# Optimization experiments

Hardware: AMD Instinct MI355X
Metric: run time of the kernel (lower is better)

## Reference

```python
import jax, jax.numpy as jnp
import numpy as np

D_MODEL = 1024
N_HEADS = 16
SEQ_LEN = 2048
BATCH = 2
NEG = -1.0e9


def sinusoidal_embeddings(seq_len, d_k):
    # Faithful to the torch version: row 0 is all zeros; even cols get sin,
    # odd cols get cos of position/theta (theta uses the SAME index j, not j//2).
    theta = 10000.0 ** (2.0 * jnp.arange(d_k, dtype=jnp.float32) / d_k)  # [d_k]
    pos = jnp.arange(1, seq_len, dtype=jnp.float32)[:, None] / theta      # [S-1, d_k]
    even = (jnp.arange(d_k) % 2 == 0)
    body = jnp.where(even, jnp.sin(pos), jnp.cos(pos))                    # [S-1, d_k]
    return jnp.concatenate([jnp.zeros((1, d_k), dtype=pos.dtype), body], axis=0)


def setup_inputs() -> dict:
    key = jax.random.key(0)
    k_x, k_q, k_k, k_v, k_o = jax.random.split(key, 5)
    scale = 0.02
    return {
        "X": jax.random.normal(k_x, (BATCH, SEQ_LEN, D_MODEL), dtype=jnp.float32),
        "W_q": jax.random.normal(k_q, (D_MODEL, D_MODEL), dtype=jnp.float32) * scale,
        "W_k": jax.random.normal(k_k, (D_MODEL, D_MODEL), dtype=jnp.float32) * scale,
        "W_v": jax.random.normal(k_v, (D_MODEL, D_MODEL), dtype=jnp.float32) * scale,
        "W_o": jax.random.normal(k_o, (D_MODEL, D_MODEL), dtype=jnp.float32) * scale,
    }


def reference(X, W_q, W_k, W_v, W_o):
    B, S, D = X.shape
    H, d_k = N_HEADS, D // N_HEADS

    def proj(W):  # nn.Linear (no bias): y = x @ W.T, then split heads -> [B,H,S,d_k]
        return (X @ W.T).reshape(B, S, H, d_k).transpose(0, 2, 1, 3)

    Q, K, V = proj(W_q), proj(W_k), proj(W_v)

    pos = sinusoidal_embeddings(S, d_k)          # [S, d_k]
    Q = Q + pos
    K = K + pos

    mask = jnp.triu(jnp.full((S, S), NEG, dtype=X.dtype), k=1)  # [S,S]
    scores = jnp.einsum("bhqd,bhkd->bhqk", Q, K) / jnp.sqrt(jnp.float32(d_k)) + mask
    weights = jax.nn.softmax(scores, axis=-1)
    attn = jnp.einsum("bhqk,bhkd->bhqd", weights, V)            # [B,H,S,d_k]

    attn = attn.transpose(0, 2, 1, 3).reshape(B, S, D)
    return attn @ W_o.T + X
```

## Files before the change

### kernel.cpp

```cpp
#include <hip/hip_runtime.h>
#include <hip/hip_bf16.h>
#include <math.h>

#define S_LEN 2048
#define DMODEL 1024
#define NHEADS 16
#define DHEAD 64
#define NBATCH 2
#define MROWS (NBATCH * S_LEN)

typedef float f32x4 __attribute__((ext_vector_type(4)));
typedef unsigned short u16x8 __attribute__((ext_vector_type(8)));
typedef __bf16 bf16x8 __attribute__((ext_vector_type(8)));

__device__ __forceinline__ f32x4 mfma16(u16x8 a, u16x8 b, f32x4 c) {
    return __builtin_amdgcn_mfma_f32_16x16x32_bf16(
        __builtin_bit_cast(bf16x8, a), __builtin_bit_cast(bf16x8, b), c, 0, 0, 0);
}

__device__ __forceinline__ unsigned short f2bf(float f) {
    unsigned int u = __builtin_bit_cast(unsigned int, f);
    u += 0x7FFFu + ((u >> 16) & 1u);
    return (unsigned short)(u >> 16);
}

__device__ __forceinline__ unsigned int cvtpk(float lo, float hi) {
    unsigned int r;
    asm("v_cvt_pk_bf16_f32 %0, %1, %2" : "=v"(r) : "v"(lo), "v"(hi));
    return r;
}

__device__ __forceinline__ void gl16(const void* g, void* l) {
    __builtin_amdgcn_global_load_lds(
        (const __attribute__((address_space(1))) unsigned int*)g,
        (__attribute__((address_space(3))) unsigned int*)l, 16, 0, 0);
}

__global__ __launch_bounds__(256) void cvt5(
    const float* __restrict__ X, const float* __restrict__ Wq,
    const float* __restrict__ Wk, const float* __restrict__ Wv,
    const float* __restrict__ Wo,
    unsigned short* __restrict__ Xbf, unsigned short* __restrict__ Wbf,
    float* __restrict__ pos)
{
    int b = blockIdx.x;
    if (b >= 4096) {
        int i = (b - 4096) * 256 + threadIdx.x;
        int s = i >> 6, d = i & 63;
        float theta = powf(10000.0f, (2.0f * (float)d) / 64.0f);
        float x = (float)s / theta;
        float v = (d & 1) ? cosf(x) : sinf(x);
        pos[i] = (s == 0) ? 0.0f : v;
        return;
    }
    const float* s; unsigned short* d; int t;
    if (b < 2048) { s = X; d = Xbf; t = b * 256 + threadIdx.x; }
    else {
        int z = (b - 2048) >> 9, bb = (b - 2048) & 511;
        s = (z == 0) ? Wq : (z == 1) ? Wk : (z == 2) ? Wv : Wo;
        d = Wbf + (z << 20);
        t = bb * 256 + threadIdx.x;
    }
    float4 a = *((const float4*)s + t * 2);
    float4 c = *((const float4*)s + t * 2 + 1);
    u16x8 o;
    o[0] = f2bf(a.x); o[1] = f2bf(a.y); o[2] = f2bf(a.z); o[3] = f2bf(a.w);
    o[4] = f2bf(c.x); o[5] = f2bf(c.y); o[6] = f2bf(c.z); o[7] = f2bf(c.w);
    *((u16x8*)d + t) = o;
}

__global__ __launch_bounds__(128) void gemm_qkv(
    const unsigned short* __restrict__ Xbf, const unsigned short* __restrict__ Wbf,
    const float* __restrict__ pos,
    unsigned short* __restrict__ qb, unsigned short* __restrict__ kb,
    unsigned short* __restrict__ vt)
{
    const int y = blockIdx.y;
    const int z = y >> 4;
    const unsigned short* __restrict__ W = Wbf + (z << 20);
    __shared__ unsigned short As[128 * 64];
    __shared__ unsigned short Bs[64 * 64];
    const int t = threadIdx.x;
    const int lane = t & 63;
    const int w = t >> 6;
    const int m0 = blockIdx.x * 128;
    const int n0 = (y & 15) * 64;
    const int ll = lane & 15, lg = lane >> 4;
    const int r8 = lane >> 3, ch = (lane & 7) ^ r8;

    f32x4 acc[4][4] = {};

    const unsigned short* gA[8];
    const unsigned short* gB[4];
    #pragma unroll
    for (int i = 0; i < 8; i++) gA[i] = Xbf + (m0 + w * 64 + i * 8 + r8) * 1024 + ch * 8;
    #pragma unroll
    for (int i = 0; i < 4; i++) gB[i] = W + (n0 + w * 32 + i * 8 + r8) * 1024 + ch * 8;
    unsigned short* const dA = &As[(w * 64) * 64];
    unsigned short* const dB = &Bs[(w * 32) * 64];

    const int sw0 = ((0 * 4 + lg) ^ (ll & 7)) * 16;
    const int sw1 = ((1 * 4 + lg) ^ (ll & 7)) * 16;
    const char* const pA0 = (const char*)As + (w * 64 + ll) * 128 + sw0;
    const char* const pA1 = (const char*)As + (w * 64 + ll) * 128 + sw1;
    const char* const pB0 = (const char*)Bs + ll * 128 + sw0;
    const char* const pB1 = (const char*)Bs + ll * 128 + sw1;

    for (int k0 = 0; k0 < 1024; k0 += 64) {
        __syncthreads();
        #pragma unroll
        for (int i = 0; i < 8; i++) { gl16(gA[i], dA + i * 8 * 64); gA[i] += 64; }
        #pragma unroll
        for (int i = 0; i < 4; i++) { gl16(gB[i], dB + i * 8 * 64); gB[i] += 64; }
        __syncthreads();
        u16x8 af[4], bfv[4];
        #pragma unroll
        for (int m = 0; m < 4; m++) af[m] = *(const u16x8*)(pA0 + m * 2048);
        #pragma unroll
        for (int n = 0; n < 4; n++) bfv[n] = *(const u16x8*)(pB0 + n * 2048);
        __builtin_amdgcn_s_setprio(1);
        #pragma unroll
        for (int m = 0; m < 4; m++)
            #pragma unroll
            for (int n = 0; n < 4; n++)
                acc[m][n] = mfma16(af[m], bfv[n], acc[m][n]);
        __builtin_amdgcn_s_setprio(0);
        #pragma unroll
        for (int m = 0; m < 4; m++) af[m] = *(const u16x8*)(pA1 + m * 2048);
        #pragma unroll
        for (int n = 0; n < 4; n++) bfv[n] = *(const u16x8*)(pB1 + n * 2048);
        __builtin_amdgcn_s_setprio(1);
        #pragma unroll
        for (int m = 0; m < 4; m++)
            #pragma unroll
            for (int n = 0; n < 4; n++)
                acc[m][n] = mfma16(af[m], bfv[n], acc[m][n]);
        __builtin_amdgcn_s_setprio(0);
    }

    if (z == 2) {
        #pragma unroll
        for (int m = 0; m < 4; m++) {
            const int row0 = m0 + w * 64 + m * 16 + lg * 4;
            const int b = row0 >> 11, s0 = row0 & 2047;
            #pragma unroll
            for (int n = 0; n < 4; n++) {
                const int c = n0 + n * 16 + ll;
                const int h = c >> 6, d = c & 63;
                unsigned long long pk =
                    (unsigned long long)cvtpk(acc[m][n][0], acc[m][n][1]) |
                    ((unsigned long long)cvtpk(acc[m][n][2], acc[m][n][3]) << 32);
                *(unsigned long long*)&vt[(((b * NHEADS + h) * 64) + d) * S_LEN + s0] = pk;
            }
        }
    } else {
        unsigned short* const dst = (z == 0) ? qb : kb;
        #pragma unroll
        for (int m = 0; m < 4; m++) {
            #pragma unroll
            for (int n = 0; n < 4; n++) {
                #pragma unroll
                for (int r = 0; r < 4; r++) {
                    const int row = m0 + w * 64 + m * 16 + lg * 4 + r;
                    const int c = n0 + n * 16 + ll;
                    const int b = row >> 11, s = row & 2047;
                    const int h = c >> 6, d = c & 63;
                    float v = acc[m][n][r] + pos[s * 64 + d];
                    if (z == 0) v *= 0.1803368801111244f;
                    dst[(((b * NHEADS + h) * S_LEN) + s) * 64 + d] = f2bf(v);
                }
            }
        }
    }
}

__global__ __launch_bounds__(512, 4) void attn_kernel(
    const unsigned short* __restrict__ qb,
    const unsigned short* __restrict__ kb,
    const unsigned short* __restrict__ vt,
    unsigned short* __restrict__ attnb)
{
    __shared__ unsigned short Klds[2][64 * 64];
    __shared__ unsigned short Vlds[2][64 * 64];
    __shared__ unsigned short Plds[8][16 * 64];

    const int bh = blockIdx.y;
    const int x = blockIdx.x;
    const int qt = (bh < 16) ? (15 - x) : x;

    const int lane = threadIdx.x & 63;
    const int w = threadIdx.x >> 6;
    const int lg = lane >> 4, ll = lane & 15;
    const int r8 = lane >> 3, ch = (lane & 7) ^ r8;

    const unsigned short* Q = qb + bh * (S_LEN * 64);
    const unsigned short* K = kb + bh * (S_LEN * 64);
    const unsigned short* V = vt + bh * (64 * S_LEN);
    const int q0 = qt * 128 + w * 16;

    u16x8 qf0 = *(const u16x8*)(Q + (q0 + ll) * 64 + lg * 8);
    u16x8 qf1 = *(const u16x8*)(Q + (q0 + ll) * 64 + 32 + lg * 8);

    f32x4 o_acc[4] = {};
    float l_part = 0.0f;

    const int sw0 = ((0 * 4 + lg) ^ (ll & 7)) * 16;
    const int sw1 = ((1 * 4 + lg) ^ (ll & 7)) * 16;
    const int llb = ll * 128;
    const char* k0p0 = (const char*)&Klds[0][0] + llb + sw0;
    const char* k0p1 = (const char*)&Klds[0][0] + llb + sw1;
    const char* k1p0 = (const char*)&Klds[1][0] + llb + sw0;
    const char* k1p1 = (const char*)&Klds[1][0] + llb + sw1;
    const char* v0p0 = (const char*)&Vlds[0][0] + llb + sw0;
    const char* v0p1 = (const char*)&Vlds[0][0] + llb + sw1;
    const char* v1p0 = (const char*)&Vlds[1][0] + llb + sw0;
    const char* v1p1 = (const char*)&Vlds[1][0] + llb + sw1;
    const int E = (ll & 7) << 4;
    char* pwb = (char*)&Plds[w][0] + ((llb + lg * 8) ^ (E & 16));
    const int pw_o0 = 0 ^ (E & 96), pw_o1 = 32 ^ (E & 96);
    const int pw_o2 = 64 ^ (E & 96), pw_o3 = 96 ^ (E & 96);
    const char* pr0 = (const char*)&Plds[w][0] + llb + sw0;
    const char* pr1 = (const char*)&Plds[w][0] + llb + sw1;
    unsigned short* kd0 = &Klds[0][(w * 8) * 64];
    unsigned short* kd1 = &Klds[1][(w * 8) * 64];
    unsigned short* vd0 = &Vlds[0][(w * 8) * 64];
    unsigned short* vd1 = &Vlds[1][(w * 8) * 64];
    const unsigned short* gk = K + (w * 8 + r8) * 64 + ch * 8;
    const unsigned short* gv = V + (w * 8 + r8) * S_LEN + ch * 8;
    const int dthr = w * 16 + ll - lg * 4;

    auto stage2 = [&](unsigned short* kd, unsigned short* vd) {
        gl16(gk, kd);
        gl16(gv, vd);
        gk += 64 * 64;
        gv += 64;
    };

    auto tile_body = [&](const char* kp0, const char* kp1,
                         const char* vp0, const char* vp1, bool masked, int thr) {
        f32x4 sc[4] = {};
        __builtin_amdgcn_s_setprio(1);
        #pragma unroll
        for (int f = 0; f < 4; f++) {
            const u16x8 kfa = *(const u16x8*)(kp0 + f * 2048);
            sc[f] = mfma16(kfa, qf0, sc[f]);
            const u16x8 kfb = *(const u16x8*)(kp1 + f * 2048);
            sc[f] = mfma16(kfb, qf1, sc[f]);
        }
        __builtin_amdgcn_s_setprio(0);
        if (masked) {
            #pragma unroll
            for (int f = 0; f < 4; f++)
                #pragma unroll
                for (int r = 0; r < 4; r++)
                    if (f * 16 + r > thr) sc[f][r] = -1.0e9f;
        }
        float ts = 0.0f;
        #pragma unroll
        for (int f = 0; f < 4; f++)
            #pragma unroll
            for (int r = 0; r < 4; r++) {
                const float p = __builtin_amdgcn_exp2f(sc[f][r]);
                sc[f][r] = p;
                ts += p;
            }
        l_part += ts;
        *(unsigned long long*)(pwb + pw_o0) =
            (unsigned long long)cvtpk(sc[0][0], sc[0][1]) | ((unsigned long long)cvtpk(sc[0][2], sc[0][3]) << 32);
        *(unsigned long long*)(pwb + pw_o1) =
            (unsigned long long)cvtpk(sc[1][0], sc[1][1]) | ((unsigned long long)cvtpk(sc[1][2], sc[1][3]) << 32);
        *(unsigned long long*)(pwb + pw_o2) =
            (unsigned long long)cvtpk(sc[2][0], sc[2][1]) | ((unsigned long long)cvtpk(sc[2][2], sc[2][3]) << 32);
        *(unsigned long long*)(pwb + pw_o3) =
            (unsigned long long)cvtpk(sc[3][0], sc[3][1]) | ((unsigned long long)cvtpk(sc[3][2], sc[3][3]) << 32);
        const u16x8 pf0 = *(const u16x8*)pr0;
        const u16x8 pf1 = *(const u16x8*)pr1;
        __builtin_amdgcn_s_setprio(1);
        #pragma unroll
        for (int f = 0; f < 4; f++) {
            o_acc[f] = mfma16(pf0, *(const u16x8*)(vp0 + f * 2048), o_acc[f]);
            o_acc[f] = mfma16(pf1, *(const u16x8*)(vp1 + f * 2048), o_acc[f]);
        }
        __builtin_amdgcn_s_setprio(0);
    };

    stage2(kd0, vd0);

    for (int p = 0; p < qt; p++) {
        __syncthreads();
        stage2(kd1, vd1);
        tile_body(k0p0, k0p1, v0p0, v0p1, false, 0);
        __syncthreads();
        stage2(kd0, vd0);
        tile_body(k1p0, k1p1, v1p0, v1p1, false, 0);
    }
    __syncthreads();
    stage2(kd1, vd1);
    tile_body(k0p0, k0p1, v0p0, v0p1, true, dthr);
    __syncthreads();
    if (w >= 4)
        tile_body(k1p0, k1p1, v1p0, v1p1, true, dthr - 64);

    l_part += __shfl_xor(l_part, 16);
    l_part += __shfl_xor(l_part, 32);

    const int bb = bh >> 4, h = bh & 15;
    float lr0 = 1.0f / __shfl(l_part, lg * 4 + 0);
    float lr1 = 1.0f / __shfl(l_part, lg * 4 + 1);
    float lr2 = 1.0f / __shfl(l_part, lg * 4 + 2);
    float lr3 = 1.0f / __shfl(l_part, lg * 4 + 3);
    #pragma unroll
    for (int f = 0; f < 4; f++) {
        const int colbase = h * 64 + f * 16 + ll;
        attnb[(bb * S_LEN + q0 + lg * 4 + 0) * DMODEL + colbase] = f2bf(o_acc[f][0] * lr0);
        attnb[(bb * S_LEN + q0 + lg * 4 + 1) * DMODEL + colbase] = f2bf(o_acc[f][1] * lr1);
        attnb[(bb * S_LEN + q0 + lg * 4 + 2) * DMODEL + colbase] = f2bf(o_acc[f][2] * lr2);
        attnb[(bb * S_LEN + q0 + lg * 4 + 3) * DMODEL + colbase] = f2bf(o_acc[f][3] * lr3);
    }
}

__global__ __launch_bounds__(256) void gemm_out(
    const unsigned short* __restrict__ Abf,
    const unsigned short* __restrict__ Wbf,
    const float* __restrict__ X,
    float* __restrict__ out)
{
    const unsigned short* __restrict__ W = Wbf + (3u << 20);
    __shared__ unsigned short As[128 * 64];
    __shared__ unsigned short Bs[128 * 64];
    const int t = threadIdx.x;
    const int lane = t & 63;
    const int w = t >> 6, wr = w >> 1, wc = w & 1;
    const int m0 = blockIdx.x * 128;
    const int n0 = blockIdx.y * 128;
    const int ll = lane & 15, lg = lane >> 4;
    const int r8 = lane >> 3, ch = (lane & 7) ^ r8;

    f32x4 acc[4][4] = {};

    const unsigned short* gA[4];
    const unsigned short* gB[4];
    #pragma unroll
    for (int c = 0; c < 4; c++) {
        gA[c] = Abf + (m0 + c * 32 + w * 8 + r8) * 1024 + ch * 8;
        gB[c] = W + (n0 + c * 32 + w * 8 + r8) * 1024 + ch * 8;
    }
    const int sw0 = ((0 * 4 + lg) ^ (ll & 7)) * 16;
    const int sw1 = ((1 * 4 + lg) ^ (ll & 7)) * 16;
    const char* const pA0 = (const char*)As + (wr * 64 + ll) * 128 + sw0;
    const char* const pA1 = (const char*)As + (wr * 64 + ll) * 128 + sw1;
    const char* const pB0 = (const char*)Bs + (wc * 64 + ll) * 128 + sw0;
    const char* const pB1 = (const char*)Bs + (wc * 64 + ll) * 128 + sw1;

    for (int k0 = 0; k0 < 1024; k0 += 64) {
        __syncthreads();
        #pragma unroll
        for (int c = 0; c < 4; c++) {
            gl16(gA[c], &As[(c * 32 + w * 8) * 64]); gA[c] += 64;
            gl16(gB[c], &Bs[(c * 32 + w * 8) * 64]); gB[c] += 64;
        }
        __syncthreads();
        u16x8 af[4], bfv[4];
        #pragma unroll
        for (int m = 0; m < 4; m++) af[m] = *(const u16x8*)(pA0 + m * 2048);
        #pragma unroll
        for (int n = 0; n < 4; n++) bfv[n] = *(const u16x8*)(pB0 + n * 2048);
        __builtin_amdgcn_s_setprio(1);
        #pragma unroll
        for (int m = 0; m < 4; m++)
            #pragma unroll
            for (int n = 0; n < 4; n++)
                acc[m][n] = mfma16(af[m], bfv[n], acc[m][n]);
        __builtin_amdgcn_s_setprio(0);
        #pragma unroll
        for (int m = 0; m < 4; m++) af[m] = *(const u16x8*)(pA1 + m * 2048);
        #pragma unroll
        for (int n = 0; n < 4; n++) bfv[n] = *(const u16x8*)(pB1 + n * 2048);
        __builtin_amdgcn_s_setprio(1);
        #pragma unroll
        for (int m = 0; m < 4; m++)
            #pragma unroll
            for (int n = 0; n < 4; n++)
                acc[m][n] = mfma16(af[m], bfv[n], acc[m][n]);
        __builtin_amdgcn_s_setprio(0);
    }

    #pragma unroll
    for (int m = 0; m < 4; m++)
        #pragma unroll
        for (int n = 0; n < 4; n++)
            #pragma unroll
            for (int r = 0; r < 4; r++) {
                int row = m0 + wr * 64 + m * 16 + lg * 4 + r;
                int col = n0 + wc * 64 + n * 16 + ll;
                out[row * 1024 + col] = acc[m][n][r] + X[row * 1024 + col];
            }
}

extern "C" void kernel_launch(void* const* d_in, const int* in_sizes, int n_in,
                              void* d_out, int out_size, void* d_ws, size_t ws_size,
                              hipStream_t stream) {
    const float* X  = (const float*)d_in[0];
    const float* Wq = (const float*)d_in[1];
    const float* Wk = (const float*)d_in[2];
    const float* Wv = (const float*)d_in[3];
    const float* Wo = (const float*)d_in[4];
    float* out = (float*)d_out;

    char* ws = (char*)d_ws;
    float*          pos  = (float*)(ws);
    unsigned short* Xbf  = (unsigned short*)(ws + (512u << 10));
    unsigned short* Wbf  = (unsigned short*)(ws + (512u << 10) + (8u  << 20));
    unsigned short* qb   = (unsigned short*)(ws + (512u << 10) + (16u << 20));
    unsigned short* kb   = (unsigned short*)(ws + (512u << 10) + (24u << 20));
    unsigned short* vt   = (unsigned short*)(ws + (512u << 10) + (32u << 20));
    unsigned short* attb = Xbf;

    cvt5<<<dim3(4608), dim3(256), 0, stream>>>(X, Wq, Wk, Wv, Wo, Xbf, Wbf, pos);
    gemm_qkv<<<dim3(32, 48), dim3(128), 0, stream>>>(Xbf, Wbf, pos, qb, kb, vt);
    attn_kernel<<<dim3(16, 32), dim3(512), 0, stream>>>(qb, kb, vt, attb);
    gemm_out<<<dim3(32, 8), dim3(256), 0, stream>>>(attb, Wbf, X, out);
}
```

Baseline: 110.4 us.

## Triple-buffer LDS with async prefetch in QKV and output GEMMs

Both GEMMs now use a three-stage LDS ring filled by global_load_lds, with vmcnt-based waits so loads for the next two K tiles overlap the MFMA work on the current one. This removes the double __syncthreads per K step that exposed global-load latency. gemm_out is also retiled to 128x64 tiles with 128 threads, matching gemm_qkv and doubling its grid to 512 blocks. The cost is more LDS per block (72 KB), which may limit how many blocks fit on each CU.

```diff
diff --git a/kernel.cpp b/kernel.cpp
--- a/kernel.cpp
+++ b/kernel.cpp
@@ -35,6 +35,17 @@
         (const __attribute__((address_space(1))) unsigned int*)g,
         (__attribute__((address_space(3))) unsigned int*)l, 16, 0, 0);
 }
+
+#define PIPE_BAR_12() do { \
+    asm volatile("s_waitcnt vmcnt(12)" ::: "memory"); \
+    __builtin_amdgcn_sched_barrier(0); \
+    __builtin_amdgcn_s_barrier(); \
+    __builtin_amdgcn_sched_barrier(0); } while (0)
+#define PIPE_BAR_0() do { \
+    asm volatile("s_waitcnt vmcnt(0)" ::: "memory"); \
+    __builtin_amdgcn_sched_barrier(0); \
+    __builtin_amdgcn_s_barrier(); \
+    __builtin_amdgcn_sched_barrier(0); } while (0)
 
 __global__ __launch_bounds__(256) void cvt5(
     const float* __restrict__ X, const float* __restrict__ Wq,
@@ -78,8 +89,7 @@
     const int y = blockIdx.y;
     const int z = y >> 4;
     const unsigned short* __restrict__ W = Wbf + (z << 20);
-    __shared__ unsigned short As[128 * 64];
-    __shared__ unsigned short Bs[64 * 64];
+    __shared__ unsigned short L[3][192 * 64];
     const int t = threadIdx.x;
     const int lane = t & 63;
     const int w = t >> 6;
@@ -96,23 +106,23 @@
     for (int i = 0; i < 8; i++) gA[i] = Xbf + (m0 + w * 64 + i * 8 + r8) * 1024 + ch * 8;
     #pragma unroll
     for (int i = 0; i < 4; i++) gB[i] = W + (n0 + w * 32 + i * 8 + r8) * 1024 + ch * 8;
-    unsigned short* const dA = &As[(w * 64) * 64];
-    unsigned short* const dB = &Bs[(w * 32) * 64];
 
     const int sw0 = ((0 * 4 + lg) ^ (ll & 7)) * 16;
     const int sw1 = ((1 * 4 + lg) ^ (ll & 7)) * 16;
-    const char* const pA0 = (const char*)As + (w * 64 + ll) * 128 + sw0;
-    const char* const pA1 = (const char*)As + (w * 64 + ll) * 128 + sw1;
-    const char* const pB0 = (const char*)Bs + ll * 128 + sw0;
-    const char* const pB1 = (const char*)Bs + ll * 128 + sw1;
-
-    for (int k0 = 0; k0 < 1024; k0 += 64) {
-        __syncthreads();
+
+    auto stage = [&](unsigned short* Lb) {
+        unsigned short* const dA = Lb + (w * 64) * 64;
+        unsigned short* const dB = Lb + 128 * 64 + (w * 32) * 64;
         #pragma unroll
         for (int i = 0; i < 8; i++) { gl16(gA[i], dA + i * 8 * 64); gA[i] += 64; }
         #pragma unroll
         for (int i = 0; i < 4; i++) { gl16(gB[i], dB + i * 8 * 64); gB[i] += 64; }
-        __syncthreads();
+    };
+    auto compute = [&](const unsigned short* Lb) {
+        const char* const pA0 = (const char*)Lb + (w * 64 + ll) * 128 + sw0;
+        const char* const pA1 = (const char*)Lb + (w * 64 + ll) * 128 + sw1;
+        const char* const pB0 = (const char*)Lb + 16384 + ll * 128 + sw0;
+        const char* const pB1 = (const char*)Lb + 16384 + ll * 128 + sw1;
         u16x8 af[4], bfv[4];
         #pragma unroll
         for (int m = 0; m < 4; m++) af[m] = *(const u16x8*)(pA0 + m * 2048);
@@ -136,7 +146,20 @@
             for (int n = 0; n < 4; n++)
                 acc[m][n] = mfma16(af[m], bfv[n], acc[m][n]);
         __builtin_amdgcn_s_setprio(0);
-    }
+    };
+
+    stage(L[0]);
+    stage(L[1]);
+    PIPE_BAR_12();
+    for (int tt = 0; tt < 4; tt++) {
+        stage(L[2]); compute(L[0]); PIPE_BAR_12();
+        stage(L[0]); compute(L[1]); PIPE_BAR_12();
+        stage(L[1]); compute(L[2]); PIPE_BAR_12();
+    }
+    stage(L[2]); compute(L[0]); PIPE_BAR_12();
+    stage(L[0]); compute(L[1]); PIPE_BAR_12();
+    compute(L[2]); PIPE_BAR_0();
+    compute(L[0]);
 
     if (z == 2) {
         #pragma unroll
@@ -319,47 +342,47 @@
     }
 }
 
-__global__ __launch_bounds__(256) void gemm_out(
+__global__ __launch_bounds__(128) void gemm_out(
     const unsigned short* __restrict__ Abf,
     const unsigned short* __restrict__ Wbf,
     const float* __restrict__ X,
     float* __restrict__ out)
 {
     const unsigned short* __restrict__ W = Wbf + (3u << 20);
-    __shared__ unsigned short As[128 * 64];
-    __shared__ unsigned short Bs[128 * 64];
+    __shared__ unsigned short L[3][192 * 64];
     const int t = threadIdx.x;
     const int lane = t & 63;
-    const int w = t >> 6, wr = w >> 1, wc = w & 1;
+    const int w = t >> 6;
     const int m0 = blockIdx.x * 128;
-    const int n0 = blockIdx.y * 128;
+    const int n0 = blockIdx.y * 64;
     const int ll = lane & 15, lg = lane >> 4;
     const int r8 = lane >> 3, ch = (lane & 7) ^ r8;
 
     f32x4 acc[4][4] = {};
 
-    const unsigned short* gA[4];
+    const unsigned short* gA[8];
     const unsigned short* gB[4];
     #pragma unroll
-    for (int c = 0; c < 4; c++) {
-        gA[c] = Abf + (m0 + c * 32 + w * 8 + r8) * 1024 + ch * 8;
-        gB[c] = W + (n0 + c * 32 + w * 8 + r8) * 1024 + ch * 8;
-    }
+    for (int i = 0; i < 8; i++) gA[i] = Abf + (m0 + w * 64 + i * 8 + r8) * 1024 + ch * 8;
+    #pragma unroll
+    for (int i = 0; i < 4; i++) gB[i] = W + (n0 + w * 32 + i * 8 + r8) * 1024 + ch * 8;
+
     const int sw0 = ((0 * 4 + lg) ^ (ll & 7)) * 16;
     const int sw1 = ((1 * 4 + lg) ^ (ll & 7)) * 16;
-    const char* const pA0 = (const char*)As + (wr * 64 + ll) * 128 + sw0;
-    const char* const pA1 = (const char*)As + (wr * 64 + ll) * 128 + sw1;
-    const char* const pB0 = (const char*)Bs + (wc * 64 + ll) * 128 + sw0;
-    const char* const pB1 = (const char*)Bs + (wc * 64 + ll) * 128 + sw1;
-
-    for (int k0 = 0; k0 < 1024; k0 += 64) {
-        __syncthreads();
-        #pragma unroll
-        for (int c = 0; c < 4; c++) {
-            gl16(gA[c], &As[(c * 32 + w * 8) * 64]); gA[c] += 64;
-            gl16(gB[c], &Bs[(c * 32 + w * 8) * 64]); gB[c] += 64;
-        }
-        __syncthreads();
+
+    auto stage = [&](unsigned short* Lb) {
+        unsigned short* const dA = Lb + (w * 64) * 64;
+        unsigned short* const dB = Lb + 128 * 64 + (w * 32) * 64;
+        #pragma unroll
+        for (int i = 0; i < 8; i++) { gl16(gA[i], dA + i * 8 * 64); gA[i] += 64; }
+        #pragma unroll
+        for (int i = 0; i < 4; i++) { gl16(gB[i], dB + i * 8 * 64); gB[i] += 64; }
+    };
+    auto compute = [&](const unsigned short* Lb) {
+        const char* const pA0 = (const char*)Lb + (w * 64 + ll) * 128 + sw0;
+        const char* const pA1 = (const char*)Lb + (w * 64 + ll) * 128 + sw1;
+        const char* const pB0 = (const char*)Lb + 16384 + ll * 128 + sw0;
+        const char* const pB1 = (const char*)Lb + 16384 + ll * 128 + sw1;
         u16x8 af[4], bfv[4];
         #pragma unroll
         for (int m = 0; m < 4; m++) af[m] = *(const u16x8*)(pA0 + m * 2048);
@@ -383,7 +406,20 @@
             for (int n = 0; n < 4; n++)
                 acc[m][n] = mfma16(af[m], bfv[n], acc[m][n]);
         __builtin_amdgcn_s_setprio(0);
-    }
+    };
+
+    stage(L[0]);
+    stage(L[1]);
+    PIPE_BAR_12();
+    for (int tt = 0; tt < 4; tt++) {
+        stage(L[2]); compute(L[0]); PIPE_BAR_12();
+        stage(L[0]); compute(L[1]); PIPE_BAR_12();
+        stage(L[1]); compute(L[2]); PIPE_BAR_12();
+    }
+    stage(L[2]); compute(L[0]); PIPE_BAR_12();
+    stage(L[0]); compute(L[1]); PIPE_BAR_12();
+    compute(L[2]); PIPE_BAR_0();
+    compute(L[0]);
 
     #pragma unroll
     for (int m = 0; m < 4; m++)
@@ -391,8 +427,8 @@
         for (int n = 0; n < 4; n++)
             #pragma unroll
             for (int r = 0; r < 4; r++) {
-                int row = m0 + wr * 64 + m * 16 + lg * 4 + r;
-                int col = n0 + wc * 64 + n * 16 + ll;
+                const int row = m0 + w * 64 + m * 16 + lg * 4 + r;
+                const int col = n0 + n * 16 + ll;
                 out[row * 1024 + col] = acc[m][n][r] + X[row * 1024 + col];
             }
 }
@@ -419,5 +455,5 @@
     cvt5<<<dim3(4608), dim3(256), 0, stream>>>(X, Wq, Wk, Wv, Wo, Xbf, Wbf, pos);
     gemm_qkv<<<dim3(32, 48), dim3(128), 0, stream>>>(Xbf, Wbf, pos, qb, kb, vt);
     attn_kernel<<<dim3(16, 32), dim3(512), 0, stream>>>(qb, kb, vt, attb);
-    gemm_out<<<dim3(32, 8), dim3(256), 0, stream>>>(attb, Wbf, X, out);
-}
+    gemm_out<<<dim3(32, 16), dim3(128), 0, stream>>>(attb, Wbf, X, out);
+}
```

Result: faster. 102.4 us (-7.3%).
